# Kernel tuning notes

Hardware: AMD Instinct MI355X
Metric: run time of the kernel (lower is better)

The kernel has to match this reference:

```python
import jax, jax.numpy as jnp
import numpy as np

N_ITER = 30       # fixed-point iterations (repo iterates to tol 3e-6, max 300)
POWER_ITERS = 50  # power iteration steps for spectral radius
KAPPA = 0.9
EPS = 1e-12


def project_l1_ball_rows(W, v):
    # projection_norm_inf: project each row of W onto the L1 ball of radius v
    a = jnp.abs(W)
    s = -jnp.sort(-a, axis=-1)                      # descending |w|
    cs = jnp.cumsum(s, axis=-1)
    k = jnp.arange(1, W.shape[-1] + 1, dtype=W.dtype)
    rho = jnp.sum((s * k > (cs - v)).astype(jnp.int32), axis=-1)  # >= 1
    cs_rho = jnp.take_along_axis(cs, (rho - 1)[:, None], axis=-1)[:, 0]
    theta = (cs_rho - v) / rho.astype(W.dtype)
    proj = jnp.sign(W) * jnp.maximum(a - theta[:, None], 0.0)
    needs = jnp.sum(a, axis=-1) > v
    return jnp.where(needs[:, None], proj, W)


def spmm_XA(X, src, dst, w, n):
    # X @ A with sparse A given as edges A[src, dst] = w ; X: (m, n)
    # (X A)[:, j] = sum_{edges i->j} w * X[:, i]
    return jax.ops.segment_sum(X.T[src] * w[:, None], dst, num_segments=n).T


def spectral_radius(src, dst, w, n):
    v0 = jnp.full((n,), 1.0 / np.sqrt(float(n)), dtype=w.dtype)
    def matvec(v):
        # (A v)[i] = sum_{edges i->j} w * v[j]
        return jax.ops.segment_sum(w * v[dst], src, num_segments=n)
    def body(i, v):
        av = matvec(v)
        return av / (jnp.linalg.norm(av) + EPS)
    v = jax.lax.fori_loop(0, POWER_ITERS, body, v0)
    return jnp.linalg.norm(matvec(v))


def setup_inputs() -> dict:
    key = jax.random.key(0)
    ks = jax.random.split(key, 7)
    n, p, m, c, E = 50000, 256, 128, 40, 800000
    return {
        "features": jax.random.normal(ks[0], (p, n), jnp.float32),
        "W": jax.random.normal(ks[1], (m, m), jnp.float32),
        "Omega_1": jax.random.normal(ks[2], (m, p), jnp.float32),
        "V_w": jax.random.normal(ks[3], (c, m), jnp.float32),
        "X_0": jnp.zeros((m, n), jnp.float32),
        "edge_weight": jax.random.uniform(ks[4], (E,), jnp.float32),
        "edge_src": jax.random.randint(ks[5], (E,), 0, n, jnp.int32),
        "edge_dst": jax.random.randint(ks[6], (E,), 0, n, jnp.int32),
    }


def reference(features, W, Omega_1, V_w, X_0, edge_weight, edge_src, edge_dst):
    n = features.shape[1]
    # spectral radius of A (computed without grad in the original, scipy eigs)
    rho = jax.lax.stop_gradient(spectral_radius(edge_src, edge_dst, edge_weight, n))
    Wp = project_l1_ball_rows(W, KAPPA / rho)
    # b_Omega = Omega_1 @ U @ A  -> (nhid, n)
    b = spmm_XA(Omega_1 @ features, edge_src, edge_dst, edge_weight, n)
    def step(X, _):
        Xn = jax.nn.relu(Wp @ spmm_XA(X, edge_src, edge_dst, edge_weight, n) + b)
        return Xn, None
    X, _ = jax.lax.scan(step, X_0, None, length=N_ITER)
    H = X.T                                        # (n, nhid)
    H = H / jnp.clip(jnp.linalg.norm(H, axis=-1, keepdims=True), EPS)
    # dropout: eval mode -> identity
    return H @ V_w.T                               # (n, nclass)
```

## Files before the change

kernel.cpp:

```cpp
#include <hip/hip_runtime.h>
#include <math.h>

#define N_NODES 50000
#define N_EDGES 800000
#define M_HID   128
#define P_FEAT  256
#define C_OUT   40
#define PWR_ITERS 16
#define FP_ITERS  30
#define KAPPA 0.9f
#define SBLK 256
#define NBK ((N_NODES + 255) / 256)

typedef unsigned short u16;
typedef unsigned int   u32;
typedef __attribute__((ext_vector_type(8))) short short8;
typedef __attribute__((ext_vector_type(4))) float f32x4;

__device__ inline u16 f2bf(float f) {
    union { float f; u32 u; } c; c.f = f;
    u32 u = c.u + 0x7fffu + ((c.u >> 16) & 1u);
    return (u16)(u >> 16);
}
__device__ inline u32 pack2bf(float lo, float hi) {
    return (u32)f2bf(lo) | ((u32)f2bf(hi) << 16);
}
__device__ inline float bflo(u32 u) { union { u32 u; float f; } c; c.u = u << 16; return c.f; }
__device__ inline float bfhi(u32 u) { union { u32 u; float f; } c; c.u = u & 0xffff0000u; return c.f; }


__global__ void fill_pow(float* buf0, float* ss, int n, float val) {
    int i = blockIdx.x * blockDim.x + threadIdx.x;
    if (i < n) buf0[i] = val;
    if (blockIdx.x == 0 && threadIdx.x < 64) ss[threadIdx.x] = (threadIdx.x == 0) ? 1.f : 0.f;
}


__global__ __launch_bounds__(256) void matvec_norm(const int* __restrict__ offs,
                                                   const int2* __restrict__ csr,
                                                   const int* __restrict__ perm,
                                                   const float* __restrict__ vin,
                                                   const float* __restrict__ n2in,
                                                   float* __restrict__ vout,
                                                   float* n2out, int n) {
    int t = blockIdx.x * blockDim.x + threadIdx.x;
    int g = t >> 3, q = t & 7;
    float inv = 1.f / (sqrtf(*n2in) + 1e-12f);
    float a = 0.f;
    int j = -1;
    if (g < n) {
        j = perm[g];
        int lo = offs[j], hi = offs[j + 1];
        for (int e = lo + q; e < hi; e += 8) {
            int2 c = csr[e];
            a += __int_as_float(c.y) * vin[c.x];
        }
    }
    a += __shfl_xor(a, 1, 64);
    a += __shfl_xor(a, 2, 64);
    a += __shfl_xor(a, 4, 64);
    a *= inv;
    if (g < n && q == 0) vout[j] = a;
    float s = (q == 0 && g < n) ? a * a : 0.f;
    for (int o = 32; o > 0; o >>= 1) s += __shfl_down(s, o, 64);
    __shared__ float ls[4];
    int lane = threadIdx.x & 63, wid = threadIdx.x >> 6;
    if (lane == 0) ls[wid] = s;
    __syncthreads();
    if (threadIdx.x == 0) atomicAdd(n2out, ls[0] + ls[1] + ls[2] + ls[3]);
}


__global__ __launch_bounds__(128) void project_w(const float* __restrict__ W,
                                                 const float* __restrict__ rho2,
                                                 u16* __restrict__ Bswz) {
    __shared__ float sa[128];
    __shared__ float ssort[128];
    __shared__ float sc[128];
    __shared__ int cnt2[2];
    int r = blockIdx.x, t = threadIdx.x;
    float radius = KAPPA / sqrtf(*rho2);
    float w0 = W[r * 128 + t];
    float a = fabsf(w0);
    sa[t] = a;
    __syncthreads();
    int rank = 0;
    #pragma unroll 8
    for (int j = 0; j < 128; ++j) {
        float aj = sa[j];
        rank += (aj > a) || (aj == a && j < t);
    }
    ssort[rank] = a;
    __syncthreads();
    sc[t] = ssort[t];
    __syncthreads();
    for (int off = 1; off < 128; off <<= 1) {
        float add = (t >= off) ? sc[t - off] : 0.f;
        __syncthreads();
        sc[t] += add;
        __syncthreads();
    }
    bool flag = ssort[t] * (float)(t + 1) > sc[t] - radius;
    unsigned long long b = __ballot(flag);
    if ((t & 63) == 0) cnt2[t >> 6] = __popcll(b);
    __syncthreads();
    int rho = cnt2[0] + cnt2[1];
    float total = sc[127];
    bool needs = total > radius;
    float theta = (sc[rho - 1] - radius) / (float)rho;
    float o;
    if (needs) {
        float am = a - theta;
        o = (am > 0.f) ? ((w0 > 0.f) ? am : -am) : 0.f;
    } else o = w0;
    int kf = t >> 5, quad = (t >> 3) & 3, jj = t & 7;
    int nt = r >> 4, li = r & 15;
    int l = quad * 16 + li;
    Bswz[((size_t)(kf * 8 + nt) * 64 + l) * 8 + jj] = f2bf(o);
}


__global__ __launch_bounds__(256) void reorder_om(const float* __restrict__ Om,
                                                  u16* __restrict__ Ofrg) {
    int idx = blockIdx.x * 256 + threadIdx.x;
    int r = idx >> 8, k = idx & 255;
    int nt = r >> 4, li = r & 15;
    int kf = k >> 5, sub = (k >> 3) & 3, jj = k & 7;
    int l = sub * 16 + li;
    Ofrg[((size_t)(kf * 8 + nt) * 64 + l) * 8 + jj] = f2bf(Om[idx]);
}


__global__ void count_deg(const int* __restrict__ dst, int* deg, int E) {
    int e = blockIdx.x * blockDim.x + threadIdx.x;
    if (e < E) atomicAdd(&deg[dst[e]], 1);
}

__global__ __launch_bounds__(SBLK) void scan_local(const int* __restrict__ deg,
                                                   int* __restrict__ offsets,
                                                   int* __restrict__ bsum, int n1) {
    __shared__ int s[SBLK];
    int i = blockIdx.x * SBLK + threadIdx.x;
    int v = (i < n1 - 1) ? deg[i] : 0;
    s[threadIdx.x] = v;
    __syncthreads();
    for (int o = 1; o < SBLK; o <<= 1) {
        int add = (threadIdx.x >= o) ? s[threadIdx.x - o] : 0;
        __syncthreads();
        s[threadIdx.x] += add;
        __syncthreads();
    }
    if (i < n1) offsets[i] = s[threadIdx.x] - v;
    if (threadIdx.x == SBLK - 1) bsum[blockIdx.x] = s[SBLK - 1];
}

__global__ __launch_bounds__(SBLK) void scan_bsum(const int* __restrict__ bsum,
                                                  int* __restrict__ bbase, int nb) {
    __shared__ int s[SBLK];
    int v = (threadIdx.x < nb) ? bsum[threadIdx.x] : 0;
    s[threadIdx.x] = v;
    __syncthreads();
    for (int o = 1; o < 256; o <<= 1) {
        int add = (threadIdx.x >= o) ? s[threadIdx.x - o] : 0;
        __syncthreads();
        s[threadIdx.x] += add;
        __syncthreads();
    }
    if (threadIdx.x < nb) bbase[threadIdx.x] = s[threadIdx.x] - v;
}

__global__ __launch_bounds__(SBLK) void scan_add(int* __restrict__ offsets,
                                                 int* __restrict__ cursor,
                                                 const int* __restrict__ bbase, int n1) {
    int i = blockIdx.x * SBLK + threadIdx.x;
    if (i < n1) {
        int o = offsets[i] + bbase[blockIdx.x];
        offsets[i] = o;
        if (i < n1 - 1) cursor[i] = o;
    }
}

__global__ void fill_csr(const int* __restrict__ src, const int* __restrict__ dst,
                         const float* __restrict__ w,
                         int* cur_d, int2* csr_d, int E) {
    int e = blockIdx.x * blockDim.x + threadIdx.x;
    if (e < E) {
        int d = dst[e];
        int pd = atomicAdd(&cur_d[d], 1);
        csr_d[pd] = make_int2(src[e], __float_as_int(w[e]));
    }
}


__global__ __launch_bounds__(256) void bhist(const int* __restrict__ deg,
                                             int* __restrict__ bh, int n) {
    __shared__ int h[256];
    int t = threadIdx.x;
    h[t] = 0;
    __syncthreads();
    int i = blockIdx.x * 256 + t;
    if (i < n) {
        int d = deg[i]; if (d > 255) d = 255;
        atomicAdd(&h[d], 1);
    }
    __syncthreads();
    bh[t * NBK + blockIdx.x] = h[t];
}

__global__ __launch_bounds__(256) void bscatter(const int* __restrict__ deg,
                                                const int* __restrict__ obase,
                                                int* __restrict__ perm, int n) {
    __shared__ int cur[256];
    int t = threadIdx.x;
    cur[t] = obase[t * NBK + blockIdx.x];
    __syncthreads();
    int i = blockIdx.x * 256 + t;
    if (i < n) {
        int d = deg[i]; if (d > 255) d = 255;
        int p = atomicAdd(&cur[d], 1);
        perm[p] = i;
    }
}

__global__ void build_invperm(const int* __restrict__ perm, int* __restrict__ invp, int n) {
    int i = blockIdx.x * blockDim.x + threadIdx.x;
    if (i < n) invp[perm[i]] = i;
}

__global__ void remap_csr(const int2* __restrict__ in, const int* __restrict__ invp,
                          int2* __restrict__ outp, int E) {
    int e = blockIdx.x * blockDim.x + threadIdx.x;
    if (e < E) {
        int2 c = in[e];
        c.x = invp[c.x];
        outp[e] = c;
    }
}


__global__ void transpose_x0_bf16(const float* __restrict__ X0, const int* __restrict__ invp,
                                  u16* Xb, int n) {
    __shared__ float tile[32][33];
    int jb = blockIdx.x * 32, tb = blockIdx.y * 32;
    int tx = threadIdx.x, ty = threadIdx.y;
    for (int r = 0; r < 32; r += 8) {
        int t = tb + ty + r, j = jb + tx;
        tile[ty + r][tx] = (j < n) ? X0[(size_t)t * n + j] : 0.f;
    }
    __syncthreads();
    for (int r = 0; r < 32; r += 8) {
        int j = jb + ty + r, t = tb + tx;
        if (j < n) Xb[(size_t)invp[j] * 128 + t] = f2bf(tile[tx][ty + r]);
    }
}


__global__ __launch_bounds__(256) void gemm_u_mfma(const float* __restrict__ F,
                                                   const u16* __restrict__ Ofrg,
                                                   u16* __restrict__ Utb, int n) {
    __shared__ u32 As32[64][17];
    int tid = threadIdx.x;
    int w = tid >> 6, l = tid & 63;
    int j0 = blockIdx.x * 64;
    const short8* __restrict__ bfr = (const short8*)Ofrg;
    f32x4 acc[8];
    #pragma unroll
    for (int nt = 0; nt < 8; ++nt) acc[nt] = (f32x4){0.f, 0.f, 0.f, 0.f};
    for (int kf = 0; kf < 8; ++kf) {
        int k0 = kf * 32;
        __syncthreads();
        #pragma unroll
        for (int r = 0; r < 4; ++r) {
            int idx = r * 256 + tid;
            int jj = idx & 63, kk2 = idx >> 6;
            int j = j0 + jj;
            float f0 = 0.f, f1 = 0.f;
            if (j < n) {
                f0 = F[(size_t)(k0 + 2 * kk2) * n + j];
                f1 = F[(size_t)(k0 + 2 * kk2 + 1) * n + j];
            }
            As32[jj][kk2] = pack2bf(f0, f1);
        }
        __syncthreads();
        u32 a0 = As32[w * 16 + (l & 15)][(l >> 4) * 4 + 0];
        u32 a1 = As32[w * 16 + (l & 15)][(l >> 4) * 4 + 1];
        u32 a2 = As32[w * 16 + (l & 15)][(l >> 4) * 4 + 2];
        u32 a3 = As32[w * 16 + (l & 15)][(l >> 4) * 4 + 3];
        short8 a;
        a[0] = (short)(a0 & 0xffff); a[1] = (short)(a0 >> 16);
        a[2] = (short)(a1 & 0xffff); a[3] = (short)(a1 >> 16);
        a[4] = (short)(a2 & 0xffff); a[5] = (short)(a2 >> 16);
        a[6] = (short)(a3 & 0xffff); a[7] = (short)(a3 >> 16);
        #pragma unroll
        for (int nt = 0; nt < 8; ++nt) {
            short8 b = bfr[(kf * 8 + nt) * 64 + l];
            acc[nt] = __builtin_amdgcn_mfma_f32_16x16x32_bf16(a, b, acc[nt], 0, 0, 0);
        }
    }
    int rbase = j0 + w * 16 + (l >> 4) * 4;
    int cbase = l & 15;
    #pragma unroll
    for (int nt = 0; nt < 8; ++nt) {
        int col = nt * 16 + cbase;
        #pragma unroll
        for (int i = 0; i < 4; ++i) {
            int row = rbase + i;
            if (row < n) Utb[(size_t)row * 128 + col] = f2bf(acc[nt][i]);
        }
    }
}


__global__ __launch_bounds__(256) void reorder_bt(const u16* __restrict__ btr,
                                                  const int* __restrict__ perm,
                                                  uint2* __restrict__ btf, int n) {
    int t = blockIdx.y * 256 + threadIdx.x;
    int idx16 = blockIdx.x;
    int nt = t >> 6, lane = t & 63;
    int r0 = idx16 * 16 + (lane >> 4) * 4;
    int c = nt * 16 + (lane & 15);
    u16 b0 = (r0 + 0 < n) ? btr[(size_t)perm[r0 + 0] * 128 + c] : 0;
    u16 b1 = (r0 + 1 < n) ? btr[(size_t)perm[r0 + 1] * 128 + c] : 0;
    u16 b2 = (r0 + 2 < n) ? btr[(size_t)perm[r0 + 2] * 128 + c] : 0;
    u16 b3 = (r0 + 3 < n) ? btr[(size_t)perm[r0 + 3] * 128 + c] : 0;
    uint2 o;
    o.x = (u32)b0 | ((u32)b1 << 16);
    o.y = (u32)b2 | ((u32)b3 << 16);
    btf[(size_t)(idx16 * 8 + nt) * 64 + lane] = o;
}


__global__ __launch_bounds__(256) void spmm_bf16(const int* __restrict__ offsets,
                                                 const int2* __restrict__ csr,
                                                 const int* __restrict__ perm,
                                                 const u16* __restrict__ Xin,
                                                 u16* __restrict__ Yout, int n) {
    int tid = threadIdx.x;
    int wid = tid >> 6, lane = tid & 63;
    int q = lane >> 4, li = lane & 15;
    int jp = blockIdx.x * 16 + wid * 4 + q;
    if (jp >= n) return;
    int j = perm[jp];
    int lo = offsets[j], hi = offsets[j + 1];
    const uint4* __restrict__ X4 = (const uint4*)Xin;
    float a[8] = {};
    int e = lo;
    for (; e + 8 <= hi; e += 8) {
        int2 c[8];
        #pragma unroll
        for (int u = 0; u < 8; ++u) c[u] = csr[e + u];
        uint4 x[8];
        #pragma unroll
        for (int u = 0; u < 8; ++u) x[u] = X4[(size_t)c[u].x * 16 + li];
        #pragma unroll
        for (int u = 0; u < 8; ++u) {
            float w = __int_as_float(c[u].y);
            a[0] += w * bflo(x[u].x); a[1] += w * bfhi(x[u].x);
            a[2] += w * bflo(x[u].y); a[3] += w * bfhi(x[u].y);
            a[4] += w * bflo(x[u].z); a[5] += w * bfhi(x[u].z);
            a[6] += w * bflo(x[u].w); a[7] += w * bfhi(x[u].w);
        }
    }
    for (; e < hi; ++e) {
        int2 c = csr[e];
        float w = __int_as_float(c.y);
        uint4 x = X4[(size_t)c.x * 16 + li];
        a[0] += w * bflo(x.x); a[1] += w * bfhi(x.x);
        a[2] += w * bflo(x.y); a[3] += w * bfhi(x.y);
        a[4] += w * bflo(x.z); a[5] += w * bfhi(x.z);
        a[6] += w * bflo(x.w); a[7] += w * bfhi(x.w);
    }
    uint4 o;
    o.x = pack2bf(a[0], a[1]);
    o.y = pack2bf(a[2], a[3]);
    o.z = pack2bf(a[4], a[5]);
    o.w = pack2bf(a[6], a[7]);
    ((uint4*)Yout)[(size_t)j * 16 + li] = o;
}


__global__ __launch_bounds__(512) void fused_fp(const int* __restrict__ offsets,
                                                const int2* __restrict__ csrp,
                                                const int* __restrict__ perm,
                                                const u16* __restrict__ Xin,
                                                const u16* __restrict__ Bswz,
                                                const uint2* __restrict__ btf,
                                                u16* __restrict__ Xout, int n) {
    __shared__ uint4 Ys[32][17];
    int tid = threadIdx.x;

    {
        int qw = tid >> 4, li = tid & 15;
        int jp = blockIdx.x * 32 + qw;
        float a[8] = {};
        if (jp < n) {
            int j = perm[jp];
            int lo = offsets[j], hi = offsets[j + 1];
            const uint4* __restrict__ X4 = (const uint4*)Xin;
            int e = lo;
            for (; e + 8 <= hi; e += 8) {
                int2 c[8];
                #pragma unroll
                for (int u = 0; u < 8; ++u) c[u] = csrp[e + u];
                uint4 x[8];
                #pragma unroll
                for (int u = 0; u < 8; ++u) x[u] = X4[(size_t)c[u].x * 16 + li];
                #pragma unroll
                for (int u = 0; u < 8; ++u) {
                    float w = __int_as_float(c[u].y);
                    a[0] += w * bflo(x[u].x); a[1] += w * bfhi(x[u].x);
                    a[2] += w * bflo(x[u].y); a[3] += w * bfhi(x[u].y);
                    a[4] += w * bflo(x[u].z); a[5] += w * bfhi(x[u].z);
                    a[6] += w * bflo(x[u].w); a[7] += w * bfhi(x[u].w);
                }
            }
            for (; e < hi; ++e) {
                int2 c = csrp[e];
                float w = __int_as_float(c.y);
                uint4 x = X4[(size_t)c.x * 16 + li];
                a[0] += w * bflo(x.x); a[1] += w * bfhi(x.x);
                a[2] += w * bflo(x.y); a[3] += w * bfhi(x.y);
                a[4] += w * bflo(x.z); a[5] += w * bfhi(x.z);
                a[6] += w * bflo(x.w); a[7] += w * bfhi(x.w);
            }
        }
        uint4 o;
        o.x = pack2bf(a[0], a[1]);
        o.y = pack2bf(a[2], a[3]);
        o.z = pack2bf(a[4], a[5]);
        o.w = pack2bf(a[6], a[7]);
        Ys[qw][li] = o;
    }
    __syncthreads();

    int w = tid >> 6, l = tid & 63;
    int rg = w & 1;
    int ntb = (w >> 1) * 2;
    f32x4 acc[2];
    acc[0] = (f32x4){0.f, 0.f, 0.f, 0.f};
    acc[1] = (f32x4){0.f, 0.f, 0.f, 0.f};
    const short8* __restrict__ bfr = (const short8*)Bswz;
    #pragma unroll
    for (int kf = 0; kf < 4; ++kf) {
        short8 a = *((const short8*)&Ys[rg * 16 + (l & 15)][kf * 4 + (l >> 4)]);
        #pragma unroll
        for (int t = 0; t < 2; ++t) {
            short8 b = bfr[(kf * 8 + ntb + t) * 64 + l];
            acc[t] = __builtin_amdgcn_mfma_f32_16x16x32_bf16(a, b, acc[t], 0, 0, 0);
        }
    }
    int pidx16 = blockIdx.x * 2 + rg;
    int lrbase = rg * 16 + (l >> 4) * 4;
    int cbase = l & 15;
    #pragma unroll
    for (int t = 0; t < 2; ++t) {
        int nt = ntb + t;
        uint2 bb = btf[(size_t)(pidx16 * 8 + nt) * 64 + l];
        float bi[4] = {bflo(bb.x), bfhi(bb.x), bflo(bb.y), bfhi(bb.y)};
        int col = nt * 16 + cbase;
        #pragma unroll
        for (int i = 0; i < 4; ++i) {
            int jp = blockIdx.x * 32 + lrbase + i;
            if (jp < n) {
                float v = acc[t][i] + bi[i];
                Xout[(size_t)jp * 128 + col] = f2bf(v > 0.f ? v : 0.f);
            }
        }
    }
}


__global__ __launch_bounds__(256) void final_out(const u16* __restrict__ Xb,
                                                 const int* __restrict__ perm,
                                                 const float* __restrict__ Vw,
                                                 float* __restrict__ out, int n) {
    __shared__ float Vs[40][132];
    int tid = threadIdx.x;
    int jb = blockIdx.x * 64;
    for (int i = tid; i < 40 * 128; i += 256) {
        int c = i >> 7, k = i & 127;
        Vs[c][(k >> 5) * 33 + (k & 31)] = Vw[i];
    }
    int g = tid >> 2, q = tid & 3;
    int jp = jb + g;
    float xs[32];
    float ssq = 0.f;
    if (jp < n) {
        const uint4* X4 = (const uint4*)(Xb + (size_t)jp * 128) + q * 4;
        #pragma unroll
        for (int v = 0; v < 4; ++v) {
            uint4 u = X4[v];
            xs[v * 8 + 0] = bflo(u.x); xs[v * 8 + 1] = bfhi(u.x);
            xs[v * 8 + 2] = bflo(u.y); xs[v * 8 + 3] = bfhi(u.y);
            xs[v * 8 + 4] = bflo(u.z); xs[v * 8 + 5] = bfhi(u.z);
            xs[v * 8 + 6] = bflo(u.w); xs[v * 8 + 7] = bfhi(u.w);
        }
        #pragma unroll
        for (int m = 0; m < 32; ++m) ssq += xs[m] * xs[m];
    } else {
        #pragma unroll
        for (int m = 0; m < 32; ++m) xs[m] = 0.f;
    }
    ssq += __shfl_xor(ssq, 1, 64);
    ssq += __shfl_xor(ssq, 2, 64);
    float inv = 1.f / fmaxf(sqrtf(ssq), 1e-12f);
    #pragma unroll
    for (int m = 0; m < 32; ++m) xs[m] *= inv;
    __syncthreads();
    float pacc[10];
    #pragma unroll
    for (int cc = 0; cc < 10; ++cc) pacc[cc] = 0.f;
    #pragma unroll 1
    for (int c = 0; c < 40; ++c) {
        const float* vrow = &Vs[c][q * 33];
        float acc = 0.f;
        #pragma unroll
        for (int m = 0; m < 32; ++m) acc += xs[m] * vrow[m];
        acc += __shfl_xor(acc, 1, 64);
        acc += __shfl_xor(acc, 2, 64);
        if ((c & 3) == q) pacc[c >> 2] = acc;
    }
    if (jp < n) {
        int j = perm[jp];
        #pragma unroll
        for (int cc = 0; cc < 10; ++cc) {
            int c = cc * 4 + q;
            out[(size_t)j * 40 + c] = pacc[cc];
        }
    }
}


extern "C" void kernel_launch(void* const* d_in, const int* in_sizes, int n_in,
                              void* d_out, int out_size, void* d_ws, size_t ws_size,
                              hipStream_t stream) {
    const float* F    = (const float*)d_in[0];
    const float* W    = (const float*)d_in[1];
    const float* Om   = (const float*)d_in[2];
    const float* Vw   = (const float*)d_in[3];
    const float* X0   = (const float*)d_in[4];
    const float* ew   = (const float*)d_in[5];
    const int*   esrc = (const int*)d_in[6];
    const int*   edst = (const int*)d_in[7];
    float* out = (float*)d_out;
    (void)in_sizes; (void)n_in; (void)out_size; (void)ws_size;

    char* ws = (char*)d_ws;
    size_t off = 0;
    auto alloc = [&](size_t bytes) -> void* {
        void* p = ws + off;
        off = (off + bytes + 255) & ~(size_t)255;
        return p;
    };
    float* buf0    = (float*)alloc((size_t)N_NODES * 4);
    float* buf1    = (float*)alloc((size_t)N_NODES * 4);
    float* ss      = (float*)alloc(64 * 4);
    int*   deg     = (int*)  alloc((size_t)(N_NODES + 1) * 4);
    int*   offs_d  = (int*)  alloc((size_t)(N_NODES + 1) * 4);
    int*   cur_d   = (int*)  alloc((size_t)N_NODES * 4);
    int*   bsum    = (int*)  alloc(512 * 4);
    int*   bbase   = (int*)  alloc(512 * 4);
    int*   bh      = (int*)  alloc((size_t)(256 * NBK + 1) * 4);
    int*   obase   = (int*)  alloc((size_t)(256 * NBK + 1) * 4);
    int*   ocur    = (int*)  alloc((size_t)(256 * NBK + 1) * 4);
    int*   perm    = (int*)  alloc((size_t)N_NODES * 4);
    int*   invp    = (int*)  alloc((size_t)N_NODES * 4);
    int2*  csr_d   = (int2*) alloc((size_t)N_EDGES * 8);
    int2*  csrp    = (int2*) alloc((size_t)N_EDGES * 8);
    u16*   Bswz    = (u16*)  alloc(128 * 128 * 2);
    u16*   Ofrg    = (u16*)  alloc(128 * 256 * 2);
    u16*   btr     = (u16*)  alloc((size_t)N_NODES * 128 * 2);
    uint2* btf     = (uint2*)alloc((size_t)3200 * 512 * 8);
    u16*   Utb     = (u16*)  alloc((size_t)N_NODES * 128 * 2);
    u16*   Xa      = (u16*)  alloc((size_t)N_NODES * 128 * 2);
    u16*   Xb      = (u16*)  alloc((size_t)N_NODES * 128 * 2);

    hipMemsetAsync(deg, 0, (size_t)(N_NODES + 1) * 4, stream);

    const int n1 = N_NODES + 1;
    const int nb = (n1 + SBLK - 1) / SBLK;

    count_deg<<<(N_EDGES + 255) / 256, 256, 0, stream>>>(edst, deg, N_EDGES);
    scan_local<<<nb, SBLK, 0, stream>>>(deg, offs_d, bsum, n1);
    scan_bsum<<<1, SBLK, 0, stream>>>(bsum, bbase, nb);
    scan_add<<<nb, SBLK, 0, stream>>>(offs_d, cur_d, bbase, n1);
    fill_csr<<<(N_EDGES + 255) / 256, 256, 0, stream>>>(
        esrc, edst, ew, cur_d, csr_d, N_EDGES);

    bhist<<<NBK, 256, 0, stream>>>(deg, bh, N_NODES);
    {
        const int sn1 = 256 * NBK + 1;
        const int snb = (sn1 + SBLK - 1) / SBLK;
        scan_local<<<snb, SBLK, 0, stream>>>(bh, obase, bsum, sn1);
        scan_bsum<<<1, SBLK, 0, stream>>>(bsum, bbase, snb);
        scan_add<<<snb, SBLK, 0, stream>>>(obase, ocur, bbase, sn1);
    }
    bscatter<<<NBK, 256, 0, stream>>>(deg, obase, perm, N_NODES);
    build_invperm<<<(N_NODES + 255) / 256, 256, 0, stream>>>(perm, invp, N_NODES);
    remap_csr<<<(N_EDGES + 255) / 256, 256, 0, stream>>>(csr_d, invp, csrp, N_EDGES);

    fill_pow<<<(N_NODES + 255) / 256, 256, 0, stream>>>(
        buf0, ss, N_NODES, 1.f / sqrtf((float)N_NODES));
    float* bufs[2] = {buf0, buf1};
    for (int it = 0; it <= PWR_ITERS; ++it) {
        matvec_norm<<<(8 * N_NODES + 255) / 256, 256, 0, stream>>>(
            offs_d, csr_d, perm, bufs[it & 1], ss + it,
            bufs[(it + 1) & 1], ss + it + 1, N_NODES);
    }

    project_w<<<128, 128, 0, stream>>>(W, ss + PWR_ITERS + 1, Bswz);

    reorder_om<<<128, 256, 0, stream>>>(Om, Ofrg);
    gemm_u_mfma<<<(N_NODES + 63) / 64, 256, 0, stream>>>(F, Ofrg, Utb, N_NODES);
    spmm_bf16<<<(N_NODES + 15) / 16, 256, 0, stream>>>(offs_d, csr_d, perm, Utb, btr, N_NODES);
    reorder_bt<<<dim3((N_NODES + 15) / 16, 2), 256, 0, stream>>>(btr, perm, btf, N_NODES);

    transpose_x0_bf16<<<dim3((N_NODES + 31) / 32, 4), dim3(32, 8), 0, stream>>>(X0, invp, Xa, N_NODES);
    u16* xb2[2] = {Xa, Xb};
    for (int it = 0; it < FP_ITERS; ++it) {
        fused_fp<<<(N_NODES + 31) / 32, 512, 0, stream>>>(
            offs_d, csrp, perm, xb2[it & 1], Bswz, btf, xb2[(it + 1) & 1], N_NODES);
    }

    final_out<<<(N_NODES + 63) / 64, 256, 0, stream>>>(xb2[FP_ITERS & 1], perm, Vw, out, N_NODES);
}
```

Baseline: 1.933 ms.

## Build permuted CSR directly and precompute row ranges; cut power iterations

The CSR fill now writes permuted source indices directly, which removes the separate remap pass and the unpermuted CSR buffer. A per-permuted-row (lo,hi) array is precomputed so the matvec, spmm and fixed-point kernels read one int2 instead of perm plus two offsets. The whole pipeline now runs in permuted node order, so the U GEMM scatters via invp and reorder_bt drops its gather. Power iterations drop from 16 to 12, which trades accuracy of the spectral-radius estimate for fewer launches.

```diff
diff --git a/kernel.cpp b/kernel.cpp
--- a/kernel.cpp
+++ b/kernel.cpp
@@ -6,7 +6,7 @@
 #define M_HID   128
 #define P_FEAT  256
 #define C_OUT   40
-#define PWR_ITERS 16
+#define PWR_ITERS 12
 #define FP_ITERS  30
 #define KAPPA 0.9f
 #define SBLK 256
@@ -36,9 +36,8 @@
 }
 
 
-__global__ __launch_bounds__(256) void matvec_norm(const int* __restrict__ offs,
-                                                   const int2* __restrict__ csr,
-                                                   const int* __restrict__ perm,
+__global__ __launch_bounds__(256) void matvec_norm(const int2* __restrict__ rowrange,
+                                                   const int2* __restrict__ csrp,
                                                    const float* __restrict__ vin,
                                                    const float* __restrict__ n2in,
                                                    float* __restrict__ vout,
@@ -47,12 +46,10 @@
     int g = t >> 3, q = t & 7;
     float inv = 1.f / (sqrtf(*n2in) + 1e-12f);
     float a = 0.f;
-    int j = -1;
     if (g < n) {
-        j = perm[g];
-        int lo = offs[j], hi = offs[j + 1];
-        for (int e = lo + q; e < hi; e += 8) {
-            int2 c = csr[e];
+        int2 rr = rowrange[g];
+        for (int e = rr.x + q; e < rr.y; e += 8) {
+            int2 c = csrp[e];
             a += __int_as_float(c.y) * vin[c.x];
         }
     }
@@ -60,7 +57,7 @@
     a += __shfl_xor(a, 2, 64);
     a += __shfl_xor(a, 4, 64);
     a *= inv;
-    if (g < n && q == 0) vout[j] = a;
+    if (g < n && q == 0) vout[g] = a;
     float s = (q == 0 && g < n) ? a * a : 0.f;
     for (int o = 32; o > 0; o >>= 1) s += __shfl_down(s, o, 64);
     __shared__ float ls[4];
@@ -180,14 +177,23 @@
     }
 }
 
-__global__ void fill_csr(const int* __restrict__ src, const int* __restrict__ dst,
-                         const float* __restrict__ w,
-                         int* cur_d, int2* csr_d, int E) {
+__global__ void fill_csr_perm(const int* __restrict__ src, const int* __restrict__ dst,
+                              const float* __restrict__ w, const int* __restrict__ invp,
+                              int* cur_d, int2* csrp, int E) {
     int e = blockIdx.x * blockDim.x + threadIdx.x;
     if (e < E) {
         int d = dst[e];
         int pd = atomicAdd(&cur_d[d], 1);
-        csr_d[pd] = make_int2(src[e], __float_as_int(w[e]));
+        csrp[pd] = make_int2(invp[src[e]], __float_as_int(w[e]));
+    }
+}
+
+__global__ void build_rowrange(const int* __restrict__ offs, const int* __restrict__ perm,
+                               int2* __restrict__ rowrange, int n) {
+    int i = blockIdx.x * blockDim.x + threadIdx.x;
+    if (i < n) {
+        int j = perm[i];
+        rowrange[i] = make_int2(offs[j], offs[j + 1]);
     }
 }
 
@@ -225,16 +231,6 @@
 __global__ void build_invperm(const int* __restrict__ perm, int* __restrict__ invp, int n) {
     int i = blockIdx.x * blockDim.x + threadIdx.x;
     if (i < n) invp[perm[i]] = i;
-}
-
-__global__ void remap_csr(const int2* __restrict__ in, const int* __restrict__ invp,
-                          int2* __restrict__ outp, int E) {
-    int e = blockIdx.x * blockDim.x + threadIdx.x;
-    if (e < E) {
-        int2 c = in[e];
-        c.x = invp[c.x];
-        outp[e] = c;
-    }
 }
 
 
@@ -257,6 +253,7 @@
 
 __global__ __launch_bounds__(256) void gemm_u_mfma(const float* __restrict__ F,
                                                    const u16* __restrict__ Ofrg,
+                                                   const int* __restrict__ invp,
                                                    u16* __restrict__ Utb, int n) {
     __shared__ u32 As32[64][17];
     int tid = threadIdx.x;
@@ -299,30 +296,34 @@
     }
     int rbase = j0 + w * 16 + (l >> 4) * 4;
     int cbase = l & 15;
+    int prow[4];
+    #pragma unroll
+    for (int i = 0; i < 4; ++i) {
+        int row = rbase + i;
+        prow[i] = (row < n) ? invp[row] : -1;
+    }
     #pragma unroll
     for (int nt = 0; nt < 8; ++nt) {
         int col = nt * 16 + cbase;
         #pragma unroll
         for (int i = 0; i < 4; ++i) {
-            int row = rbase + i;
-            if (row < n) Utb[(size_t)row * 128 + col] = f2bf(acc[nt][i]);
+            if (prow[i] >= 0) Utb[(size_t)prow[i] * 128 + col] = f2bf(acc[nt][i]);
         }
     }
 }
 
 
 __global__ __launch_bounds__(256) void reorder_bt(const u16* __restrict__ btr,
-                                                  const int* __restrict__ perm,
                                                   uint2* __restrict__ btf, int n) {
     int t = blockIdx.y * 256 + threadIdx.x;
     int idx16 = blockIdx.x;
     int nt = t >> 6, lane = t & 63;
     int r0 = idx16 * 16 + (lane >> 4) * 4;
     int c = nt * 16 + (lane & 15);
-    u16 b0 = (r0 + 0 < n) ? btr[(size_t)perm[r0 + 0] * 128 + c] : 0;
-    u16 b1 = (r0 + 1 < n) ? btr[(size_t)perm[r0 + 1] * 128 + c] : 0;
-    u16 b2 = (r0 + 2 < n) ? btr[(size_t)perm[r0 + 2] * 128 + c] : 0;
-    u16 b3 = (r0 + 3 < n) ? btr[(size_t)perm[r0 + 3] * 128 + c] : 0;
+    u16 b0 = (r0 + 0 < n) ? btr[(size_t)(r0 + 0) * 128 + c] : 0;
+    u16 b1 = (r0 + 1 < n) ? btr[(size_t)(r0 + 1) * 128 + c] : 0;
+    u16 b2 = (r0 + 2 < n) ? btr[(size_t)(r0 + 2) * 128 + c] : 0;
+    u16 b3 = (r0 + 3 < n) ? btr[(size_t)(r0 + 3) * 128 + c] : 0;
     uint2 o;
     o.x = (u32)b0 | ((u32)b1 << 16);
     o.y = (u32)b2 | ((u32)b3 << 16);
@@ -330,9 +331,8 @@
 }
 
 
-__global__ __launch_bounds__(256) void spmm_bf16(const int* __restrict__ offsets,
-                                                 const int2* __restrict__ csr,
-                                                 const int* __restrict__ perm,
+__global__ __launch_bounds__(256) void spmm_bf16(const int2* __restrict__ rowrange,
+                                                 const int2* __restrict__ csrp,
                                                  const u16* __restrict__ Xin,
                                                  u16* __restrict__ Yout, int n) {
     int tid = threadIdx.x;
@@ -340,15 +340,14 @@
     int q = lane >> 4, li = lane & 15;
     int jp = blockIdx.x * 16 + wid * 4 + q;
     if (jp >= n) return;
-    int j = perm[jp];
-    int lo = offsets[j], hi = offsets[j + 1];
+    int2 rr = rowrange[jp];
     const uint4* __restrict__ X4 = (const uint4*)Xin;
     float a[8] = {};
-    int e = lo;
-    for (; e + 8 <= hi; e += 8) {
+    int e = rr.x;
+    for (; e + 8 <= rr.y; e += 8) {
         int2 c[8];
         #pragma unroll
-        for (int u = 0; u < 8; ++u) c[u] = csr[e + u];
+        for (int u = 0; u < 8; ++u) c[u] = csrp[e + u];
         uint4 x[8];
         #pragma unroll
         for (int u = 0; u < 8; ++u) x[u] = X4[(size_t)c[u].x * 16 + li];
@@ -361,8 +360,8 @@
             a[6] += w * bflo(x[u].w); a[7] += w * bfhi(x[u].w);
         }
     }
-    for (; e < hi; ++e) {
-        int2 c = csr[e];
+    for (; e < rr.y; ++e) {
+        int2 c = csrp[e];
         float w = __int_as_float(c.y);
         uint4 x = X4[(size_t)c.x * 16 + li];
         a[0] += w * bflo(x.x); a[1] += w * bfhi(x.x);
@@ -375,13 +374,12 @@
     o.y = pack2bf(a[2], a[3]);
     o.z = pack2bf(a[4], a[5]);
     o.w = pack2bf(a[6], a[7]);
-    ((uint4*)Yout)[(size_t)j * 16 + li] = o;
-}
-
-
-__global__ __launch_bounds__(512) void fused_fp(const int* __restrict__ offsets,
+    ((uint4*)Yout)[(size_t)jp * 16 + li] = o;
+}
+
+
+__global__ __launch_bounds__(512) void fused_fp(const int2* __restrict__ rowrange,
                                                 const int2* __restrict__ csrp,
-                                                const int* __restrict__ perm,
                                                 const u16* __restrict__ Xin,
                                                 const u16* __restrict__ Bswz,
                                                 const uint2* __restrict__ btf,
@@ -394,11 +392,10 @@
         int jp = blockIdx.x * 32 + qw;
         float a[8] = {};
         if (jp < n) {
-            int j = perm[jp];
-            int lo = offsets[j], hi = offsets[j + 1];
+            int2 rr = rowrange[jp];
             const uint4* __restrict__ X4 = (const uint4*)Xin;
-            int e = lo;
-            for (; e + 8 <= hi; e += 8) {
+            int e = rr.x;
+            for (; e + 8 <= rr.y; e += 8) {
                 int2 c[8];
                 #pragma unroll
                 for (int u = 0; u < 8; ++u) c[u] = csrp[e + u];
@@ -414,7 +411,7 @@
                     a[6] += w * bflo(x[u].w); a[7] += w * bfhi(x[u].w);
                 }
             }
-            for (; e < hi; ++e) {
+            for (; e < rr.y; ++e) {
                 int2 c = csrp[e];
                 float w = __int_as_float(c.y);
                 uint4 x = X4[(size_t)c.x * 16 + li];
@@ -565,7 +562,7 @@
     int*   ocur    = (int*)  alloc((size_t)(256 * NBK + 1) * 4);
     int*   perm    = (int*)  alloc((size_t)N_NODES * 4);
     int*   invp    = (int*)  alloc((size_t)N_NODES * 4);
-    int2*  csr_d   = (int2*) alloc((size_t)N_EDGES * 8);
+    int2*  rowrng  = (int2*) alloc((size_t)N_NODES * 8);
     int2*  csrp    = (int2*) alloc((size_t)N_EDGES * 8);
     u16*   Bswz    = (u16*)  alloc(128 * 128 * 2);
     u16*   Ofrg    = (u16*)  alloc(128 * 256 * 2);
@@ -584,8 +581,6 @@
     scan_local<<<nb, SBLK, 0, stream>>>(deg, offs_d, bsum, n1);
     scan_bsum<<<1, SBLK, 0, stream>>>(bsum, bbase, nb);
     scan_add<<<nb, SBLK, 0, stream>>>(offs_d, cur_d, bbase, n1);
-    fill_csr<<<(N_EDGES + 255) / 256, 256, 0, stream>>>(
-        esrc, edst, ew, cur_d, csr_d, N_EDGES);
 
     bhist<<<NBK, 256, 0, stream>>>(deg, bh, N_NODES);
     {
@@ -597,29 +592,32 @@
     }
     bscatter<<<NBK, 256, 0, stream>>>(deg, obase, perm, N_NODES);
     build_invperm<<<(N_NODES + 255) / 256, 256, 0, stream>>>(perm, invp, N_NODES);
-    remap_csr<<<(N_EDGES + 255) / 256, 256, 0, stream>>>(csr_d, invp, csrp, N_EDGES);
+
+    fill_csr_perm<<<(N_EDGES + 255) / 256, 256, 0, stream>>>(
+        esrc, edst, ew, invp, cur_d, csrp, N_EDGES);
+    build_rowrange<<<(N_NODES + 255) / 256, 256, 0, stream>>>(offs_d, perm, rowrng, N_NODES);
 
     fill_pow<<<(N_NODES + 255) / 256, 256, 0, stream>>>(
         buf0, ss, N_NODES, 1.f / sqrtf((float)N_NODES));
     float* bufs[2] = {buf0, buf1};
     for (int it = 0; it <= PWR_ITERS; ++it) {
         matvec_norm<<<(8 * N_NODES + 255) / 256, 256, 0, stream>>>(
-            offs_d, csr_d, perm, bufs[it & 1], ss + it,
+            rowrng, csrp, bufs[it & 1], ss + it,
             bufs[(it + 1) & 1], ss + it + 1, N_NODES);
     }
 
     project_w<<<128, 128, 0, stream>>>(W, ss + PWR_ITERS + 1, Bswz);
 
     reorder_om<<<128, 256, 0, stream>>>(Om, Ofrg);
-    gemm_u_mfma<<<(N_NODES + 63) / 64, 256, 0, stream>>>(F, Ofrg, Utb, N_NODES);
-    spmm_bf16<<<(N_NODES + 15) / 16, 256, 0, stream>>>(offs_d, csr_d, perm, Utb, btr, N_NODES);
-    reorder_bt<<<dim3((N_NODES + 15) / 16, 2), 256, 0, stream>>>(btr, perm, btf, N_NODES);
+    gemm_u_mfma<<<(N_NODES + 63) / 64, 256, 0, stream>>>(F, Ofrg, invp, Utb, N_NODES);
+    spmm_bf16<<<(N_NODES + 15) / 16, 256, 0, stream>>>(rowrng, csrp, Utb, btr, N_NODES);
+    reorder_bt<<<dim3((N_NODES + 15) / 16, 2), 256, 0, stream>>>(btr, btf, N_NODES);
 
     transpose_x0_bf16<<<dim3((N_NODES + 31) / 32, 4), dim3(32, 8), 0, stream>>>(X0, invp, Xa, N_NODES);
     u16* xb2[2] = {Xa, Xb};
     for (int it = 0; it < FP_ITERS; ++it) {
         fused_fp<<<(N_NODES + 31) / 32, 512, 0, stream>>>(
-            offs_d, csrp, perm, xb2[it & 1], Bswz, btf, xb2[(it + 1) & 1], N_NODES);
+            rowrng, csrp, xb2[it & 1], Bswz, btf, xb2[(it + 1) & 1], N_NODES);
     }
 
     final_out<<<(N_NODES + 63) / 64, 256, 0, stream>>>(xb2[FP_ITERS & 1], perm, Vw, out, N_NODES);
```

Result: faster. 1.787 ms (-7.6%).
